# Kernel tuning notes

Measured on AMD Instinct MI355X. Metric: run time of the kernel, lower is better.

## Reference

```python
import jax, jax.numpy as jnp
import numpy as np

N = 4096
N_FEAT = 1024
N_HID = 8
N_HEADS = 8
N_CLASSES = 16
ALPHA = 0.2
NEG_BIG = -9e15


def setup_inputs() -> dict:
    key = jax.random.key(0)
    ks = jax.random.split(key, 6)
    x = jax.random.normal(ks[0], (N, N_FEAT), dtype=jnp.float32)
    adj = (jax.random.uniform(ks[1], (N, N)) < 0.01).astype(jnp.float32)
    adj = jnp.maximum(adj, jnp.eye(N, dtype=jnp.float32))
    W_heads = jax.random.normal(ks[2], (N_HEADS, N_FEAT, N_HID), dtype=jnp.float32) * 0.05
    a_heads = jax.random.normal(ks[3], (N_HEADS, 2 * N_HID, 1), dtype=jnp.float32) * 0.05
    W_final = jax.random.normal(ks[4], (N_HEADS * N_HID, N_CLASSES), dtype=jnp.float32) * 0.05
    a_final = jax.random.normal(ks[5], (2 * N_CLASSES, 1), dtype=jnp.float32) * 0.05
    return {"x": x, "adj": adj, "W_heads": W_heads, "a_heads": a_heads,
            "W_final": W_final, "a_final": a_final}


def gat_layer(h, adj, W, a):
    # h: [N, Fin], W: [Fin, Fout], a: [2*Fout, 1]
    Wh = h @ W                                  # [N, Fout]
    Fout = W.shape[1]
    f_src = Wh @ a[:Fout, 0]                    # [N] -- Wh_i . a[:F]
    f_dst = Wh @ a[Fout:, 0]                    # [N] -- Wh_j . a[F:]
    e = jax.nn.leaky_relu(f_src[:, None] + f_dst[None, :], ALPHA)  # [N, N]
    e = jnp.where(adj > 0, e, NEG_BIG)
    attention = jax.nn.softmax(e, axis=1)       # dropout skipped (eval mode)
    return attention @ Wh                        # [N, Fout]


def reference(x, adj, W_heads, a_heads, W_final, a_final):
    # multi-head GAT layer (8 independent heads), concat along features
    heads = jax.vmap(lambda W, a: gat_layer(x, adj, W, a))(W_heads, a_heads)  # [H, N, n_hid]
    h = jnp.transpose(heads, (1, 0, 2)).reshape(x.shape[0], -1)               # [N, H*n_hid]
    h = jax.nn.elu(h)
    out = gat_layer(h, adj, W_final, a_final)    # [N, n_classes]
    return jax.nn.log_softmax(out, axis=1)
```

## Files before the change

kernel.cpp:

```cpp
#include <hip/hip_runtime.h>
#include <math.h>

#define N 4096
#define NFEAT 1024
#define NHID 8
#define NHEADS 8
#define NCLS 16
#define CAP 128

#define GEMM_BLOCKS 512

__global__ __launch_bounds__(256) void ka_scan_gemm(const float* __restrict__ adj,
                                                    const float* __restrict__ x,
                                                    const float* __restrict__ W_heads,
                                                    const float* __restrict__ a_heads,
                                                    int* __restrict__ deg,
                                                    int* __restrict__ nbr,
                                                    float* __restrict__ Wh,
                                                    float* __restrict__ fsrc,
                                                    float* __restrict__ fdst) {
    __shared__ float smem[8 * NFEAT + 4 * 8 * 64];
    const int tid = threadIdx.x;

    if (blockIdx.x >= GEMM_BLOCKS) {
        const int row = blockIdx.x - GEMM_BLOCKS;
        int* cnt = (int*)smem;
        if (tid == 0) *cnt = 0;
        __syncthreads();
        const float4* arow = (const float4*)(adj + (size_t)row * N);
        int* outl = nbr + (size_t)row * CAP;
        float4 v[4];
        #pragma unroll
        for (int i = 0; i < 4; ++i) v[i] = arow[tid + i * 256];
        #pragma unroll
        for (int i = 0; i < 4; ++i) {
            const int b = (tid + i * 256) * 4;
            if (v[i].x > 0.f) { int p = atomicAdd(cnt, 1); if (p < CAP) outl[p] = b + 0; }
            if (v[i].y > 0.f) { int p = atomicAdd(cnt, 1); if (p < CAP) outl[p] = b + 1; }
            if (v[i].z > 0.f) { int p = atomicAdd(cnt, 1); if (p < CAP) outl[p] = b + 2; }
            if (v[i].w > 0.f) { int p = atomicAdd(cnt, 1); if (p < CAP) outl[p] = b + 3; }
        }
        __syncthreads();
        if (tid == 0) deg[row] = *cnt > CAP ? CAP : *cnt;
        return;
    }

    float* xs = smem;
    float (*red)[8][64] = (float (*)[8][64])(smem + 8 * NFEAT);
    const int w = tid >> 6, c = tid & 63;
    const int row0 = blockIdx.x * 8;

    const float4* xg = (const float4*)(x + (size_t)row0 * NFEAT);
    float4* xls = (float4*)xs;
    #pragma unroll
    for (int i = 0; i < 8; ++i) xls[tid + i * 256] = xg[tid + i * 256];
    __syncthreads();

    float acc[8] = {};
    const float* wp = W_heads + (size_t)(c >> 3) * (NFEAT * NHID) + (c & 7)
                    + (size_t)(w * 256) * NHID;
    const float* xw = xs + w * 256;
    for (int k = 0; k < 256; k += 8) {
        float wv[8];
        #pragma unroll
        for (int u = 0; u < 8; ++u) wv[u] = wp[(k + u) * 8];
        #pragma unroll
        for (int r = 0; r < 8; ++r) {
            const float4 a0 = *(const float4*)(xw + r * NFEAT + k);
            const float4 a1 = *(const float4*)(xw + r * NFEAT + k + 4);
            acc[r] += a0.x * wv[0] + a0.y * wv[1] + a0.z * wv[2] + a0.w * wv[3]
                    + a1.x * wv[4] + a1.y * wv[5] + a1.z * wv[6] + a1.w * wv[7];
        }
    }
    #pragma unroll
    for (int r = 0; r < 8; ++r) red[w][r][c] = acc[r];
    __syncthreads();
    #pragma unroll
    for (int e0 = 0; e0 < 2; ++e0) {
        int e = tid + e0 * 256;
        int r = e >> 6, cc = e & 63;
        float v = red[0][r][cc] + red[1][r][cc] + red[2][r][cc] + red[3][r][cc];
        Wh[(size_t)(row0 + r) * 64 + cc] = v;
        int h = cc >> 3, kh = cc & 7;
        float vs = v * a_heads[h * 16 + kh];
        float vd = v * a_heads[h * 16 + 8 + kh];
        vs += __shfl_xor(vs, 1); vs += __shfl_xor(vs, 2); vs += __shfl_xor(vs, 4);
        vd += __shfl_xor(vd, 1); vd += __shfl_xor(vd, 2); vd += __shfl_xor(vd, 4);
        if (kh == 0) { fsrc[h * N + row0 + r] = vs; fdst[h * N + row0 + r] = vd; }
    }
}

__global__ __launch_bounds__(256) void kb_attn1(const float* __restrict__ fsrc,
                                                const float* __restrict__ fdst,
                                                const float* __restrict__ Wh,
                                                const int* __restrict__ deg,
                                                const int* __restrict__ nbr,
                                                const float* __restrict__ W_final,
                                                const float* __restrict__ a_final,
                                                float* __restrict__ Wh2,
                                                float* __restrict__ fsrc2,
                                                float* __restrict__ fdst2) {
    __shared__ float hrow[4][64];
    const int wave = threadIdx.x >> 6;
    const int lane = threadIdx.x & 63;
    const int row = blockIdx.x * 4 + wave;
    const int h = lane >> 3;
    const int d = deg[row];
    const int* nl = nbr + (size_t)row * CAP;
    const float fs = fsrc[h * N + row];
    const float* fd = fdst + h * N;

    float s = 0.f, acc = 0.f;
    int n = 0;
    for (; n + 4 <= d; n += 4) {
        int j0 = nl[n], j1 = nl[n + 1], j2 = nl[n + 2], j3 = nl[n + 3];
        float e0 = fs + fd[j0], e1 = fs + fd[j1], e2 = fs + fd[j2], e3 = fs + fd[j3];
        float v0 = Wh[(size_t)j0 * 64 + lane], v1 = Wh[(size_t)j1 * 64 + lane];
        float v2 = Wh[(size_t)j2 * 64 + lane], v3 = Wh[(size_t)j3 * 64 + lane];
        float w0 = __expf(fmaxf(e0, 0.2f * e0));
        float w1 = __expf(fmaxf(e1, 0.2f * e1));
        float w2 = __expf(fmaxf(e2, 0.2f * e2));
        float w3 = __expf(fmaxf(e3, 0.2f * e3));
        s += (w0 + w1) + (w2 + w3);
        acc += w0 * v0 + w1 * v1 + w2 * v2 + w3 * v3;
    }
    for (; n < d; ++n) {
        int j = nl[n];
        float e = fs + fd[j];
        float wgt = __expf(fmaxf(e, 0.2f * e));
        s += wgt;
        acc += wgt * Wh[(size_t)j * 64 + lane];
    }
    float o = acc / s;
    o = o > 0.f ? o : (__expf(o) - 1.f);
    hrow[wave][lane] = o;
    __syncthreads();

    const int g = lane >> 4, cc = lane & 15;
    float p = 0.f;
    #pragma unroll
    for (int f0 = 0; f0 < 16; ++f0) {
        int f = g * 16 + f0;
        p += hrow[wave][f] * W_final[f * 16 + cc];
    }
    p += __shfl_xor(p, 16);
    p += __shfl_xor(p, 32);
    if (g == 0) Wh2[(size_t)row * 16 + cc] = p;
    float vs = p * a_final[cc];
    float vd = p * a_final[16 + cc];
    #pragma unroll
    for (int mm = 1; mm < 16; mm <<= 1) {
        vs += __shfl_xor(vs, mm);
        vd += __shfl_xor(vd, mm);
    }
    if (lane == 0) { fsrc2[row] = vs; fdst2[row] = vd; }
}

__global__ __launch_bounds__(256) void kc_attn2(const float* __restrict__ fsrc2,
                                                const float* __restrict__ fdst2,
                                                const float* __restrict__ Wh2,
                                                const int* __restrict__ deg,
                                                const int* __restrict__ nbr,
                                                float* __restrict__ out) {
    const int wave = threadIdx.x >> 6;
    const int lane = threadIdx.x & 63;
    const int row = blockIdx.x * 4 + wave;
    const int jj = lane >> 4, c = lane & 15;
    const int d = deg[row];
    const int* nl = nbr + (size_t)row * CAP;
    const float fs = fsrc2[row];

    float s = 0.f, acc = 0.f;
    for (int n = jj; n < d; n += 4) {
        int j = nl[n];
        float e = fs + fdst2[j];
        float w = __expf(fmaxf(e, 0.2f * e));
        s += w;
        acc += w * Wh2[(size_t)j * 16 + c];
    }
    s += __shfl_xor(s, 16);  s += __shfl_xor(s, 32);
    acc += __shfl_xor(acc, 16); acc += __shfl_xor(acc, 32);

    float u = acc / s;
    float m2 = u;
    #pragma unroll
    for (int mm = 1; mm < 16; mm <<= 1) m2 = fmaxf(m2, __shfl_xor(m2, mm));
    float tv = u - m2;
    float se = __expf(tv);
    #pragma unroll
    for (int mm = 1; mm < 16; mm <<= 1) se += __shfl_xor(se, mm);
    float o = tv - logf(se);
    if (jj == 0) out[(size_t)row * 16 + c] = o;
}

extern "C" void kernel_launch(void* const* d_in, const int* in_sizes, int n_in,
                              void* d_out, int out_size, void* d_ws, size_t ws_size,
                              hipStream_t stream) {
    const float* x       = (const float*)d_in[0];
    const float* adj     = (const float*)d_in[1];
    const float* W_heads = (const float*)d_in[2];
    const float* a_heads = (const float*)d_in[3];
    const float* W_final = (const float*)d_in[4];
    const float* a_final = (const float*)d_in[5];
    float* out = (float*)d_out;

    float* ws    = (float*)d_ws;
    float* Wh    = ws;
    float* fsrc  = Wh + 262144;
    float* fdst  = fsrc + 32768;
    float* Wh2   = fdst + 32768;
    float* fsrc2 = Wh2 + 65536;
    float* fdst2 = fsrc2 + 4096;
    int*   deg   = (int*)(fdst2 + 4096);
    int*   nbr   = deg + 4096;

    ka_scan_gemm<<<GEMM_BLOCKS + N, 256, 0, stream>>>(adj, x, W_heads, a_heads,
                                                      deg, nbr, Wh, fsrc, fdst);
    kb_attn1    <<<N / 4, 256, 0, stream>>>(fsrc, fdst, Wh, deg, nbr,
                                            W_final, a_final, Wh2, fsrc2, fdst2);
    kc_attn2    <<<N / 4, 256, 0, stream>>>(fsrc2, fdst2, Wh2, deg, nbr, out);
}
```

Measured before the change: 137.7 us.

## Fuse second attention layer into first via per-block ready flags

Merges the two attention kernels into one, so each block publishes its Wh2/fdst2 rows and sets a per-block flag. It then spins until the flags of all blocks owning its neighbours are set before running the second-layer aggregation. This removes one kernel launch and the global barrier between them. It also reuses the x shared buffer for the reduction scratch, which shrinks LDS. The spin-waiting relies on all 1024 blocks being co-resident to avoid deadlock, and adds atomic polling traffic.

```diff
diff --git a/kernel.cpp b/kernel.cpp
--- a/kernel.cpp
+++ b/kernel.cpp
@@ -16,16 +16,18 @@
                                                     const float* __restrict__ a_heads,
                                                     int* __restrict__ deg,
                                                     int* __restrict__ nbr,
+                                                    int* __restrict__ flag,
                                                     float* __restrict__ Wh,
                                                     float* __restrict__ fsrc,
                                                     float* __restrict__ fdst) {
-    __shared__ float smem[8 * NFEAT + 4 * 8 * 64];
+    __shared__ float smem[8 * NFEAT];
     const int tid = threadIdx.x;
 
     if (blockIdx.x >= GEMM_BLOCKS) {
         const int row = blockIdx.x - GEMM_BLOCKS;
         int* cnt = (int*)smem;
         if (tid == 0) *cnt = 0;
+        if (tid == 1 && row < 1024) flag[row] = 0;
         __syncthreads();
         const float4* arow = (const float4*)(adj + (size_t)row * N);
         int* outl = nbr + (size_t)row * CAP;
@@ -46,7 +48,6 @@
     }
 
     float* xs = smem;
-    float (*red)[8][64] = (float (*)[8][64])(smem + 8 * NFEAT);
     const int w = tid >> 6, c = tid & 63;
     const int row0 = blockIdx.x * 8;
 
@@ -72,6 +73,8 @@
                     + a1.x * wv[4] + a1.y * wv[5] + a1.z * wv[6] + a1.w * wv[7];
         }
     }
+    __syncthreads();
+    float (*red)[8][64] = (float (*)[8][64])smem;
     #pragma unroll
     for (int r = 0; r < 8; ++r) red[w][r][c] = acc[r];
     __syncthreads();
@@ -90,7 +93,7 @@
     }
 }
 
-__global__ __launch_bounds__(256) void kb_attn1(const float* __restrict__ fsrc,
+__global__ __launch_bounds__(256) void kbc_attn(const float* __restrict__ fsrc,
                                                 const float* __restrict__ fdst,
                                                 const float* __restrict__ Wh,
                                                 const int* __restrict__ deg,
@@ -98,8 +101,9 @@
                                                 const float* __restrict__ W_final,
                                                 const float* __restrict__ a_final,
                                                 float* __restrict__ Wh2,
-                                                float* __restrict__ fsrc2,
-                                                float* __restrict__ fdst2) {
+                                                float* __restrict__ fdst2,
+                                                int* flag,
+                                                float* __restrict__ out) {
     __shared__ float hrow[4][64];
     const int wave = threadIdx.x >> 6;
     const int lane = threadIdx.x & 63;
@@ -153,35 +157,32 @@
         vs += __shfl_xor(vs, mm);
         vd += __shfl_xor(vd, mm);
     }
-    if (lane == 0) { fsrc2[row] = vs; fdst2[row] = vd; }
-}
-
-__global__ __launch_bounds__(256) void kc_attn2(const float* __restrict__ fsrc2,
-                                                const float* __restrict__ fdst2,
-                                                const float* __restrict__ Wh2,
-                                                const int* __restrict__ deg,
-                                                const int* __restrict__ nbr,
-                                                float* __restrict__ out) {
-    const int wave = threadIdx.x >> 6;
-    const int lane = threadIdx.x & 63;
-    const int row = blockIdx.x * 4 + wave;
-    const int jj = lane >> 4, c = lane & 15;
-    const int d = deg[row];
-    const int* nl = nbr + (size_t)row * CAP;
-    const float fs = fsrc2[row];
-
-    float s = 0.f, acc = 0.f;
-    for (int n = jj; n < d; n += 4) {
-        int j = nl[n];
-        float e = fs + fdst2[j];
+    if (lane == 0) fdst2[row] = vd;
+
+    __threadfence();
+    __syncthreads();
+    if (threadIdx.x == 0) atomicExch(&flag[blockIdx.x], 1);
+
+    for (int q = lane; q < d; q += 64) {
+        int pb = nl[q] >> 2;
+        while (atomicAdd(&flag[pb], 0) == 0) {}
+    }
+    __threadfence();
+
+    const int jj = g;
+    const float fs2 = vs;
+    float s2 = 0.f, acc2 = 0.f;
+    for (int m = jj; m < d; m += 4) {
+        int j = nl[m];
+        float e = fs2 + fdst2[j];
         float w = __expf(fmaxf(e, 0.2f * e));
-        s += w;
-        acc += w * Wh2[(size_t)j * 16 + c];
-    }
-    s += __shfl_xor(s, 16);  s += __shfl_xor(s, 32);
-    acc += __shfl_xor(acc, 16); acc += __shfl_xor(acc, 32);
-
-    float u = acc / s;
+        s2 += w;
+        acc2 += w * Wh2[(size_t)j * 16 + cc];
+    }
+    s2 += __shfl_xor(s2, 16);  s2 += __shfl_xor(s2, 32);
+    acc2 += __shfl_xor(acc2, 16); acc2 += __shfl_xor(acc2, 32);
+
+    float u = acc2 / s2;
     float m2 = u;
     #pragma unroll
     for (int mm = 1; mm < 16; mm <<= 1) m2 = fmaxf(m2, __shfl_xor(m2, mm));
@@ -189,8 +190,8 @@
     float se = __expf(tv);
     #pragma unroll
     for (int mm = 1; mm < 16; mm <<= 1) se += __shfl_xor(se, mm);
-    float o = tv - logf(se);
-    if (jj == 0) out[(size_t)row * 16 + c] = o;
+    float ov = tv - logf(se);
+    if (jj == 0) out[(size_t)row * 16 + cc] = ov;
 }
 
 extern "C" void kernel_launch(void* const* d_in, const int* in_sizes, int n_in,
@@ -209,14 +210,13 @@
     float* fsrc  = Wh + 262144;
     float* fdst  = fsrc + 32768;
     float* Wh2   = fdst + 32768;
-    float* fsrc2 = Wh2 + 65536;
-    float* fdst2 = fsrc2 + 4096;
+    float* fdst2 = Wh2 + 65536;
     int*   deg   = (int*)(fdst2 + 4096);
     int*   nbr   = deg + 4096;
+    int*   flag  = nbr + 4096 * CAP;
 
     ka_scan_gemm<<<GEMM_BLOCKS + N, 256, 0, stream>>>(adj, x, W_heads, a_heads,
-                                                      deg, nbr, Wh, fsrc, fdst);
-    kb_attn1    <<<N / 4, 256, 0, stream>>>(fsrc, fdst, Wh, deg, nbr,
-                                            W_final, a_final, Wh2, fsrc2, fdst2);
-    kc_attn2    <<<N / 4, 256, 0, stream>>>(fsrc2, fdst2, Wh2, deg, nbr, out);
+                                                      deg, nbr, flag, Wh, fsrc, fdst);
+    kbc_attn    <<<N / 4, 256, 0, stream>>>(fsrc, fdst, Wh, deg, nbr,
+                                            W_final, a_final, Wh2, fdst2, flag, out);
 }
```

New measurement: 274.4 us. 1.99x slower.

## Fuse three GAT kernels into one cooperative kernel with grid syncs

Applied to the files above, without the earlier changes.

Replaces the three-kernel pipeline (scan+GEMM, first attention, second attention) with a single cooperative kernel of 1024 blocks. Grid-wide syncs separate the phases, and each block handles 8 adjacency rows or 8 GEMM rows with smaller shared memory. The aim is to remove kernel launch gaps and tail effects between stages. In exchange, grid.sync adds its own cost and the per-block work is serialised. The fallback path also drops the 4-way unrolled neighbour loop in the first attention kernel.

```diff
diff --git a/kernel.cpp b/kernel.cpp
--- a/kernel.cpp
+++ b/kernel.cpp
@@ -1,5 +1,8 @@
 #include <hip/hip_runtime.h>
+#include <hip/hip_cooperative_groups.h>
 #include <math.h>
+
+namespace cg = cooperative_groups;
 
 #define N 4096
 #define NFEAT 1024
@@ -9,6 +12,183 @@
 #define CAP 128
 
 #define GEMM_BLOCKS 512
+#define GRID_BLOCKS 1024
+
+__global__ __launch_bounds__(256, 4) void gat_fused(const float* __restrict__ adj,
+                                                    const float* __restrict__ x,
+                                                    const float* __restrict__ W_heads,
+                                                    const float* __restrict__ a_heads,
+                                                    const float* __restrict__ W_final,
+                                                    const float* __restrict__ a_final,
+                                                    int* __restrict__ deg,
+                                                    int* __restrict__ nbr,
+                                                    float* __restrict__ Wh,
+                                                    float* __restrict__ fsrc,
+                                                    float* __restrict__ fdst,
+                                                    float* __restrict__ Wh2,
+                                                    float* __restrict__ fdst2,
+                                                    float* __restrict__ out) {
+    __shared__ float smem[4 * NFEAT];
+    const int tid = threadIdx.x;
+    cg::grid_group grid = cg::this_grid();
+
+    if (blockIdx.x >= GEMM_BLOCKS) {
+        int* cnt = (int*)smem;
+        const int rb = (blockIdx.x - GEMM_BLOCKS) * 8;
+        for (int r = 0; r < 8; ++r) {
+            const int row = rb + r;
+            if (tid == 0) *cnt = 0;
+            __syncthreads();
+            const float4* arow = (const float4*)(adj + (size_t)row * N);
+            int* outl = nbr + (size_t)row * CAP;
+            float4 v[4];
+            #pragma unroll
+            for (int i = 0; i < 4; ++i) v[i] = arow[tid + i * 256];
+            #pragma unroll
+            for (int i = 0; i < 4; ++i) {
+                const int b = (tid + i * 256) * 4;
+                if (v[i].x > 0.f) { int p = atomicAdd(cnt, 1); if (p < CAP) outl[p] = b + 0; }
+                if (v[i].y > 0.f) { int p = atomicAdd(cnt, 1); if (p < CAP) outl[p] = b + 1; }
+                if (v[i].z > 0.f) { int p = atomicAdd(cnt, 1); if (p < CAP) outl[p] = b + 2; }
+                if (v[i].w > 0.f) { int p = atomicAdd(cnt, 1); if (p < CAP) outl[p] = b + 3; }
+            }
+            __syncthreads();
+            if (tid == 0) deg[row] = *cnt > CAP ? CAP : *cnt;
+        }
+    } else {
+        const int w = tid >> 6, c = tid & 63;
+        const int row0 = blockIdx.x * 8;
+        float acc[8] = {};
+        const float* wp = W_heads + (size_t)(c >> 3) * (NFEAT * NHID) + (c & 7)
+                        + (size_t)(w * 256) * NHID;
+        for (int hh = 0; hh < 2; ++hh) {
+            __syncthreads();
+            const float4* xg = (const float4*)(x + (size_t)(row0 + hh * 4) * NFEAT);
+            float4* xls = (float4*)smem;
+            #pragma unroll
+            for (int i = 0; i < 4; ++i) xls[tid + i * 256] = xg[tid + i * 256];
+            __syncthreads();
+            const float* xw = smem + w * 256;
+            for (int k = 0; k < 256; k += 8) {
+                float wv[8];
+                #pragma unroll
+                for (int u = 0; u < 8; ++u) wv[u] = wp[(k + u) * 8];
+                #pragma unroll
+                for (int r = 0; r < 4; ++r) {
+                    const float4 a0 = *(const float4*)(xw + r * NFEAT + k);
+                    const float4 a1 = *(const float4*)(xw + r * NFEAT + k + 4);
+                    acc[hh * 4 + r] += a0.x * wv[0] + a0.y * wv[1] + a0.z * wv[2]
+                                     + a0.w * wv[3] + a1.x * wv[4] + a1.y * wv[5]
+                                     + a1.z * wv[6] + a1.w * wv[7];
+                }
+            }
+        }
+        __syncthreads();
+        float (*red)[8][64] = (float (*)[8][64])smem;
+        #pragma unroll
+        for (int r = 0; r < 8; ++r) red[w][r][c] = acc[r];
+        __syncthreads();
+        #pragma unroll
+        for (int e0 = 0; e0 < 2; ++e0) {
+            int e = tid + e0 * 256;
+            int r = e >> 6, cc = e & 63;
+            float v = red[0][r][cc] + red[1][r][cc] + red[2][r][cc] + red[3][r][cc];
+            Wh[(size_t)(row0 + r) * 64 + cc] = v;
+            int h = cc >> 3, kh = cc & 7;
+            float vs = v * a_heads[h * 16 + kh];
+            float vd = v * a_heads[h * 16 + 8 + kh];
+            vs += __shfl_xor(vs, 1); vs += __shfl_xor(vs, 2); vs += __shfl_xor(vs, 4);
+            vd += __shfl_xor(vd, 1); vd += __shfl_xor(vd, 2); vd += __shfl_xor(vd, 4);
+            if (kh == 0) { fsrc[h * N + row0 + r] = vs; fdst[h * N + row0 + r] = vd; }
+        }
+    }
+
+    grid.sync();
+
+    float* hrow = smem;
+    const int wave = tid >> 6;
+    const int lane = tid & 63;
+    const int row = blockIdx.x * 4 + wave;
+    const int h = lane >> 3;
+    const int d = deg[row];
+    const int* nl = nbr + (size_t)row * CAP;
+    {
+        const float fs = fsrc[h * N + row];
+        const float* fd = fdst + h * N;
+        float s = 0.f, acc = 0.f;
+        int n = 0;
+        for (; n + 4 <= d; n += 4) {
+            int j0 = nl[n], j1 = nl[n + 1], j2 = nl[n + 2], j3 = nl[n + 3];
+            float e0 = fs + fd[j0], e1 = fs + fd[j1], e2 = fs + fd[j2], e3 = fs + fd[j3];
+            float v0 = Wh[(size_t)j0 * 64 + lane], v1 = Wh[(size_t)j1 * 64 + lane];
+            float v2 = Wh[(size_t)j2 * 64 + lane], v3 = Wh[(size_t)j3 * 64 + lane];
+            float w0 = __expf(fmaxf(e0, 0.2f * e0));
+            float w1 = __expf(fmaxf(e1, 0.2f * e1));
+            float w2 = __expf(fmaxf(e2, 0.2f * e2));
+            float w3 = __expf(fmaxf(e3, 0.2f * e3));
+            s += (w0 + w1) + (w2 + w3);
+            acc += w0 * v0 + w1 * v1 + w2 * v2 + w3 * v3;
+        }
+        for (; n < d; ++n) {
+            int j = nl[n];
+            float e = fs + fd[j];
+            float wgt = __expf(fmaxf(e, 0.2f * e));
+            s += wgt;
+            acc += wgt * Wh[(size_t)j * 64 + lane];
+        }
+        float o = acc / s;
+        o = o > 0.f ? o : (__expf(o) - 1.f);
+        hrow[wave * 64 + lane] = o;
+    }
+    __syncthreads();
+
+    const int g = lane >> 4, cc = lane & 15;
+    float fs2;
+    {
+        float p = 0.f;
+        #pragma unroll
+        for (int f0 = 0; f0 < 16; ++f0) {
+            int f = g * 16 + f0;
+            p += hrow[wave * 64 + f] * W_final[f * 16 + cc];
+        }
+        p += __shfl_xor(p, 16);
+        p += __shfl_xor(p, 32);
+        if (g == 0) Wh2[(size_t)row * 16 + cc] = p;
+        float vs = p * a_final[cc];
+        float vd = p * a_final[16 + cc];
+        #pragma unroll
+        for (int mm = 1; mm < 16; mm <<= 1) {
+            vs += __shfl_xor(vs, mm);
+            vd += __shfl_xor(vd, mm);
+        }
+        fs2 = vs;
+        if (lane == 0) fdst2[row] = vd;
+    }
+
+    grid.sync();
+
+    float s2 = 0.f, acc2 = 0.f;
+    for (int m = g; m < d; m += 4) {
+        int j = nl[m];
+        float e = fs2 + fdst2[j];
+        float w = __expf(fmaxf(e, 0.2f * e));
+        s2 += w;
+        acc2 += w * Wh2[(size_t)j * 16 + cc];
+    }
+    s2 += __shfl_xor(s2, 16);   s2 += __shfl_xor(s2, 32);
+    acc2 += __shfl_xor(acc2, 16); acc2 += __shfl_xor(acc2, 32);
+
+    float u = acc2 / s2;
+    float m2 = u;
+    #pragma unroll
+    for (int mm = 1; mm < 16; mm <<= 1) m2 = fmaxf(m2, __shfl_xor(m2, mm));
+    float tv = u - m2;
+    float se = __expf(tv);
+    #pragma unroll
+    for (int mm = 1; mm < 16; mm <<= 1) se += __shfl_xor(se, mm);
+    float ov = tv - logf(se);
+    if (g == 0) out[(size_t)row * 16 + cc] = ov;
+}
 
 __global__ __launch_bounds__(256) void ka_scan_gemm(const float* __restrict__ adj,
                                                     const float* __restrict__ x,
@@ -19,9 +199,8 @@
                                                     float* __restrict__ Wh,
                                                     float* __restrict__ fsrc,
                                                     float* __restrict__ fdst) {
-    __shared__ float smem[8 * NFEAT + 4 * 8 * 64];
+    __shared__ float smem[8 * NFEAT];
     const int tid = threadIdx.x;
-
     if (blockIdx.x >= GEMM_BLOCKS) {
         const int row = blockIdx.x - GEMM_BLOCKS;
         int* cnt = (int*)smem;
@@ -44,18 +223,14 @@
         if (tid == 0) deg[row] = *cnt > CAP ? CAP : *cnt;
         return;
     }
-
     float* xs = smem;
-    float (*red)[8][64] = (float (*)[8][64])(smem + 8 * NFEAT);
     const int w = tid >> 6, c = tid & 63;
     const int row0 = blockIdx.x * 8;
-
     const float4* xg = (const float4*)(x + (size_t)row0 * NFEAT);
     float4* xls = (float4*)xs;
     #pragma unroll
     for (int i = 0; i < 8; ++i) xls[tid + i * 256] = xg[tid + i * 256];
     __syncthreads();
-
     float acc[8] = {};
     const float* wp = W_heads + (size_t)(c >> 3) * (NFEAT * NHID) + (c & 7)
                     + (size_t)(w * 256) * NHID;
@@ -72,6 +247,8 @@
                     + a1.x * wv[4] + a1.y * wv[5] + a1.z * wv[6] + a1.w * wv[7];
         }
     }
+    __syncthreads();
+    float (*red)[8][64] = (float (*)[8][64])smem;
     #pragma unroll
     for (int r = 0; r < 8; ++r) red[w][r][c] = acc[r];
     __syncthreads();
@@ -109,22 +286,8 @@
     const int* nl = nbr + (size_t)row * CAP;
     const float fs = fsrc[h * N + row];
     const float* fd = fdst + h * N;
-
     float s = 0.f, acc = 0.f;
-    int n = 0;
-    for (; n + 4 <= d; n += 4) {
-        int j0 = nl[n], j1 = nl[n + 1], j2 = nl[n + 2], j3 = nl[n + 3];
-        float e0 = fs + fd[j0], e1 = fs + fd[j1], e2 = fs + fd[j2], e3 = fs + fd[j3];
-        float v0 = Wh[(size_t)j0 * 64 + lane], v1 = Wh[(size_t)j1 * 64 + lane];
-        float v2 = Wh[(size_t)j2 * 64 + lane], v3 = Wh[(size_t)j3 * 64 + lane];
-        float w0 = __expf(fmaxf(e0, 0.2f * e0));
-        float w1 = __expf(fmaxf(e1, 0.2f * e1));
-        float w2 = __expf(fmaxf(e2, 0.2f * e2));
-        float w3 = __expf(fmaxf(e3, 0.2f * e3));
-        s += (w0 + w1) + (w2 + w3);
-        acc += w0 * v0 + w1 * v1 + w2 * v2 + w3 * v3;
-    }
-    for (; n < d; ++n) {
+    for (int n = 0; n < d; ++n) {
         int j = nl[n];
         float e = fs + fd[j];
         float wgt = __expf(fmaxf(e, 0.2f * e));
@@ -135,7 +298,6 @@
     o = o > 0.f ? o : (__expf(o) - 1.f);
     hrow[wave][lane] = o;
     __syncthreads();
-
     const int g = lane >> 4, cc = lane & 15;
     float p = 0.f;
     #pragma unroll
@@ -169,7 +331,6 @@
     const int d = deg[row];
     const int* nl = nbr + (size_t)row * CAP;
     const float fs = fsrc2[row];
-
     float s = 0.f, acc = 0.f;
     for (int n = jj; n < d; n += 4) {
         int j = nl[n];
@@ -180,7 +341,6 @@
     }
     s += __shfl_xor(s, 16);  s += __shfl_xor(s, 32);
     acc += __shfl_xor(acc, 16); acc += __shfl_xor(acc, 32);
-
     float u = acc / s;
     float m2 = u;
     #pragma unroll
@@ -214,9 +374,17 @@
     int*   deg   = (int*)(fdst2 + 4096);
     int*   nbr   = deg + 4096;
 
-    ka_scan_gemm<<<GEMM_BLOCKS + N, 256, 0, stream>>>(adj, x, W_heads, a_heads,
-                                                      deg, nbr, Wh, fsrc, fdst);
-    kb_attn1    <<<N / 4, 256, 0, stream>>>(fsrc, fdst, Wh, deg, nbr,
-                                            W_final, a_final, Wh2, fsrc2, fdst2);
-    kc_attn2    <<<N / 4, 256, 0, stream>>>(fsrc2, fdst2, Wh2, deg, nbr, out);
-}
+    void* args[] = {(void*)&adj, (void*)&x, (void*)&W_heads, (void*)&a_heads,
+                    (void*)&W_final, (void*)&a_final, (void*)&deg, (void*)&nbr,
+                    (void*)&Wh, (void*)&fsrc, (void*)&fdst, (void*)&Wh2,
+                    (void*)&fdst2, (void*)&out};
+    hipError_t err = hipLaunchCooperativeKernel((void*)gat_fused, dim3(GRID_BLOCKS),
+                                                dim3(256), args, 0, stream);
+    if (err != hipSuccess) {
+        ka_scan_gemm<<<GEMM_BLOCKS + N, 256, 0, stream>>>(adj, x, W_heads, a_heads,
+                                                          deg, nbr, Wh, fsrc, fdst);
+        kb_attn1    <<<N / 4, 256, 0, stream>>>(fsrc, fdst, Wh, deg, nbr,
+                                                W_final, a_final, Wh2, fsrc2, fdst2);
+        kc_attn2    <<<N / 4, 256, 0, stream>>>(fsrc2, fdst2, Wh2, deg, nbr, out);
+    }
+}
```

New measurement: 417.1 us. +202.8%, slower.

## Compute head projection GEMM with bf16 MFMA instead of fp32 FMAs

Applied to the files above, without the earlier changes.

Replaces the shared-memory fp32 GEMM of x @ W_heads with a bf16 MFMA 16x16x32 path. Each wave computes a 16x16 output tile straight from global memory, converting x and W to bf16 in registers. Rows per block grow from 8 to 16, so half as many GEMM blocks are launched and the LDS staging and cross-wave reduction go away. This cuts the compute cost of the dominant GEMM, at the price of bf16 rounding on inputs to the attention logits and uncoalesced strided W loads.

```diff
diff --git a/kernel.cpp b/kernel.cpp
--- a/kernel.cpp
+++ b/kernel.cpp
@@ -8,7 +8,16 @@
 #define NCLS 16
 #define CAP 128
 
-#define GEMM_BLOCKS 512
+#define GEMM_BLOCKS 256
+
+using bf16x8 = __attribute__((ext_vector_type(8))) short;
+using f32x4  = __attribute__((ext_vector_type(4))) float;
+
+__device__ __forceinline__ short f2bf(float f) {
+    unsigned u = __float_as_uint(f);
+    u += 0x7FFF + ((u >> 16) & 1);
+    return (short)(u >> 16);
+}
 
 __global__ __launch_bounds__(256) void ka_scan_gemm(const float* __restrict__ adj,
                                                     const float* __restrict__ x,
@@ -19,13 +28,12 @@
                                                     float* __restrict__ Wh,
                                                     float* __restrict__ fsrc,
                                                     float* __restrict__ fdst) {
-    __shared__ float smem[8 * NFEAT + 4 * 8 * 64];
+    __shared__ int cnt;
     const int tid = threadIdx.x;
 
     if (blockIdx.x >= GEMM_BLOCKS) {
         const int row = blockIdx.x - GEMM_BLOCKS;
-        int* cnt = (int*)smem;
-        if (tid == 0) *cnt = 0;
+        if (tid == 0) cnt = 0;
         __syncthreads();
         const float4* arow = (const float4*)(adj + (size_t)row * N);
         int* outl = nbr + (size_t)row * CAP;
@@ -35,58 +43,52 @@
         #pragma unroll
         for (int i = 0; i < 4; ++i) {
             const int b = (tid + i * 256) * 4;
-            if (v[i].x > 0.f) { int p = atomicAdd(cnt, 1); if (p < CAP) outl[p] = b + 0; }
-            if (v[i].y > 0.f) { int p = atomicAdd(cnt, 1); if (p < CAP) outl[p] = b + 1; }
-            if (v[i].z > 0.f) { int p = atomicAdd(cnt, 1); if (p < CAP) outl[p] = b + 2; }
-            if (v[i].w > 0.f) { int p = atomicAdd(cnt, 1); if (p < CAP) outl[p] = b + 3; }
+            if (v[i].x > 0.f) { int p = atomicAdd(&cnt, 1); if (p < CAP) outl[p] = b + 0; }
+            if (v[i].y > 0.f) { int p = atomicAdd(&cnt, 1); if (p < CAP) outl[p] = b + 1; }
+            if (v[i].z > 0.f) { int p = atomicAdd(&cnt, 1); if (p < CAP) outl[p] = b + 2; }
+            if (v[i].w > 0.f) { int p = atomicAdd(&cnt, 1); if (p < CAP) outl[p] = b + 3; }
         }
         __syncthreads();
-        if (tid == 0) deg[row] = *cnt > CAP ? CAP : *cnt;
+        if (tid == 0) deg[row] = cnt > CAP ? CAP : cnt;
         return;
     }
 
-    float* xs = smem;
-    float (*red)[8][64] = (float (*)[8][64])(smem + 8 * NFEAT);
-    const int w = tid >> 6, c = tid & 63;
-    const int row0 = blockIdx.x * 8;
-
-    const float4* xg = (const float4*)(x + (size_t)row0 * NFEAT);
-    float4* xls = (float4*)xs;
-    #pragma unroll
-    for (int i = 0; i < 8; ++i) xls[tid + i * 256] = xg[tid + i * 256];
-    __syncthreads();
-
-    float acc[8] = {};
-    const float* wp = W_heads + (size_t)(c >> 3) * (NFEAT * NHID) + (c & 7)
-                    + (size_t)(w * 256) * NHID;
-    const float* xw = xs + w * 256;
-    for (int k = 0; k < 256; k += 8) {
-        float wv[8];
+    const int lane = tid & 63;
+    const int w = tid >> 6;
+    const int m = lane & 15;
+    const int q = lane >> 4;
+    const int row0 = blockIdx.x * 16;
+    const int colw = w * 16;
+    const int c = colw + m;
+
+    f32x4 acc = {0.f, 0.f, 0.f, 0.f};
+    const float* xbase = x + (size_t)(row0 + m) * NFEAT + q * 8;
+    const float* wbase = W_heads + (size_t)(c >> 3) * (NFEAT * NHID) + (c & 7)
+                       + (size_t)(q * 8) * NHID;
+
+    for (int k0 = 0; k0 < NFEAT; k0 += 32) {
+        const float4 a0 = *(const float4*)(xbase + k0);
+        const float4 a1 = *(const float4*)(xbase + k0 + 4);
+        const float* wk = wbase + (size_t)k0 * NHID;
+        bf16x8 af, bf;
+        af[0] = f2bf(a0.x); af[1] = f2bf(a0.y); af[2] = f2bf(a0.z); af[3] = f2bf(a0.w);
+        af[4] = f2bf(a1.x); af[5] = f2bf(a1.y); af[6] = f2bf(a1.z); af[7] = f2bf(a1.w);
         #pragma unroll
-        for (int u = 0; u < 8; ++u) wv[u] = wp[(k + u) * 8];
-        #pragma unroll
-        for (int r = 0; r < 8; ++r) {
-            const float4 a0 = *(const float4*)(xw + r * NFEAT + k);
-            const float4 a1 = *(const float4*)(xw + r * NFEAT + k + 4);
-            acc[r] += a0.x * wv[0] + a0.y * wv[1] + a0.z * wv[2] + a0.w * wv[3]
-                    + a1.x * wv[4] + a1.y * wv[5] + a1.z * wv[6] + a1.w * wv[7];
-        }
-    }
-    #pragma unroll
-    for (int r = 0; r < 8; ++r) red[w][r][c] = acc[r];
-    __syncthreads();
-    #pragma unroll
-    for (int e0 = 0; e0 < 2; ++e0) {
-        int e = tid + e0 * 256;
-        int r = e >> 6, cc = e & 63;
-        float v = red[0][r][cc] + red[1][r][cc] + red[2][r][cc] + red[3][r][cc];
-        Wh[(size_t)(row0 + r) * 64 + cc] = v;
-        int h = cc >> 3, kh = cc & 7;
+        for (int j = 0; j < 8; ++j) bf[j] = f2bf(wk[j * NHID]);
+        acc = __builtin_amdgcn_mfma_f32_16x16x32_bf16(af, bf, acc, 0, 0, 0);
+    }
+
+    const int h = c >> 3, kh = m & 7;
+    #pragma unroll
+    for (int reg = 0; reg < 4; ++reg) {
+        const int r = row0 + q * 4 + reg;
+        const float v = acc[reg];
+        Wh[(size_t)r * 64 + c] = v;
         float vs = v * a_heads[h * 16 + kh];
         float vd = v * a_heads[h * 16 + 8 + kh];
         vs += __shfl_xor(vs, 1); vs += __shfl_xor(vs, 2); vs += __shfl_xor(vs, 4);
         vd += __shfl_xor(vd, 1); vd += __shfl_xor(vd, 2); vd += __shfl_xor(vd, 4);
-        if (kh == 0) { fsrc[h * N + row0 + r] = vs; fdst[h * N + row0 + r] = vd; }
+        if (kh == 0) { fsrc[h * N + r] = vs; fdst[h * N + r] = vd; }
     }
 }
 
```

After: 142.7 us. +3.6%, slower.
